# Kernel tuning notes

Hardware: AMD Instinct MI355X
Metric: run time of the kernel (lower is better)

## Reference

```python
import jax, jax.numpy as jnp
import numpy as np

SCALE_FACTOR = 2  # init kwarg
KERNEL = 1        # kernel=1 -> no Gaussian inpainting of empty cells
EPS = 1e-6


def token2map_agg(x, loc_orig, idx_agg, H, W):
    """Scatter-average aggregated tokens onto a dense [B,C,H,W] map.

    Faithful to token2map_agg_sparse with weight=None, kernel=1:
      each original position i gets feature x[idx_agg[i]] with weight 1,
      scattered to the grid cell of loc_orig[i]; per-cell average with
      denominator (count + 1e-6).
    """
    B, N, C = x.shape
    N0 = loc_orig.shape[1]
    lo = jnp.clip(loc_orig, -1.0, 1.0)
    wh = jnp.array([W, H], dtype=lo.dtype)
    # normalized [-1,1] -> pixel coords, round-half-even like torch.round
    px = jnp.round(0.5 * (lo + 1.0) * wh - 0.5).astype(jnp.int32)
    ix = jnp.clip(px[..., 0], 0, W - 1)
    iy = jnp.clip(px[..., 1], 0, H - 1)
    seg = (iy * W + ix + jnp.arange(B, dtype=jnp.int32)[:, None] * (H * W)).reshape(-1)  # [B*N0]
    # gather token feature for each original position: [B, N0, C]
    feats = jnp.take_along_axis(x, idx_agg[..., None].astype(jnp.int32), axis=1)
    # scatter features and counts together in one segment_sum
    src = jnp.concatenate([feats, jnp.ones_like(feats[..., :1])], axis=-1).reshape(B * N0, C + 1)
    agg = jax.ops.segment_sum(src, seg, num_segments=B * H * W)  # [B*H*W, C+1]
    out = agg[:, :C] / (agg[:, C:] + EPS)
    return out.reshape(B, H, W, C).transpose(0, 3, 1, 2)  # [B,C,H,W]


def setup_inputs() -> dict:
    key = jax.random.key(0)
    k1, k2, k3, k4 = jax.random.split(key, 4)
    B, N, C = 8, 1024, 128
    N0 = 16384  # 128*128 original grid positions
    x = jax.random.normal(k1, (B, N, C), dtype=jnp.float32)
    loc = jax.random.uniform(k2, (B, N, 2), dtype=jnp.float32, minval=-1.0, maxval=1.0)
    loc_orig = jax.random.uniform(k3, (B, N0, 2), dtype=jnp.float32, minval=-1.0, maxval=1.0)
    idx_agg = jax.random.randint(k4, (B, N0), 0, N, dtype=jnp.int32)
    return {"x": x, "loc": loc, "loc_orig": loc_orig, "idx_agg": idx_agg,
            "map_h": 128, "map_w": 128}


def reference(x, loc, loc_orig, idx_agg, map_h, map_w):
    B, N, C = x.shape
    N0 = idx_agg.shape[1]
    scale_orig = (N0 // N) ** 0.5  # static python value
    if SCALE_FACTOR <= scale_orig:
        h, w = int(map_h * SCALE_FACTOR), int(map_w * SCALE_FACTOR)
        out = token2map_agg(x, loc_orig, idx_agg, h, w)
    else:
        h, w = int(map_h * scale_orig), int(map_w * scale_orig)
        out = token2map_agg(x, loc_orig, idx_agg, h, w)
        h, w = int(map_h * SCALE_FACTOR), int(map_w * SCALE_FACTOR)
        out = jax.image.resize(out, (B, C, h, w), method="bilinear")
    return out
```

## Files before the change

### kernel.cpp

```cpp
#include <hip/hip_runtime.h>

constexpr int B  = 8;
constexpr int N  = 1024;
constexpr int C  = 128;
constexpr int N0 = 16384;
constexpr int HH = 256;
constexpr int WW = 256;
constexpr int HW = HH * WW;
constexpr int NPTS = B * N0;

constexpr int CPG  = 64;
constexpr int GPB  = HW / CPG;
constexpr int NGRP = B * GPB;
constexpr int CAP  = 96;

constexpr int ROW  = CPG + 4;
constexpr int ACC_WORDS = C * ROW;

__device__ __forceinline__ int cell_of(float lx, float ly) {
    lx = fminf(fmaxf(lx, -1.0f), 1.0f);
    ly = fminf(fmaxf(ly, -1.0f), 1.0f);
    float pxf = rintf(0.5f * (lx + 1.0f) * 256.0f - 0.5f);
    float pyf = rintf(0.5f * (ly + 1.0f) * 256.0f - 0.5f);
    int ix = (int)pxf; ix = ix < 0 ? 0 : (ix > WW - 1 ? WW - 1 : ix);
    int iy = (int)pyf; iy = iy < 0 ? 0 : (iy > HH - 1 ? HH - 1 : iy);
    return iy * WW + ix;
}

__global__ void bucket_kernel(const float* __restrict__ loc_orig,
                              const int* __restrict__ idx_agg,
                              int* __restrict__ cursor,
                              int* __restrict__ bucket) {
    int p = blockIdx.x * blockDim.x + threadIdx.x;
    if (p >= NPTS) return;
    float2 l = ((const float2*)loc_orig)[p];
    int b = p >> 14;
    int cell = cell_of(l.x, l.y);
    int g = b * GPB + (cell >> 6);
    int pos = atomicAdd(cursor + g, 1);
    if (pos < CAP) bucket[g * CAP + pos] = ((cell & 63) << 10) | idx_agg[p];
}

__global__ __launch_bounds__(512) void gather_kernel(
        const float* __restrict__ x,
        const int* __restrict__ cursor,
        const int* __restrict__ bucket,
        float* __restrict__ out) {
    __shared__ __align__(16) float acc[ACC_WORDS];
    __shared__ float scale[CPG];
    __shared__ int   recs[CAP];
    __shared__ int   cnt_s;

    int gid   = blockIdx.x;
    int b     = gid >> 10;
    int cell0 = (gid & 1023) * CPG;
    int tid   = threadIdx.x;
    int wave  = tid >> 6, lane = tid & 63;

    int my_cnt = (tid == 0) ? cursor[gid] : 0;
    int my_rec = (tid < CAP) ? bucket[gid * CAP + tid] : 0;

    float4 z4 = make_float4(0.f, 0.f, 0.f, 0.f);
    for (int i = tid; i < ACC_WORDS / 4; i += 512) ((float4*)acc)[i] = z4;
    if (tid < CPG) scale[tid] = 0.0f;

    if (tid == 0) cnt_s = my_cnt > CAP ? CAP : my_cnt;
    if (tid < CAP) recs[tid] = my_rec;
    __syncthreads();

    int cnt = cnt_s;

    for (int j = wave; j < cnt; j += 8) {
        int e = recs[j];
        int local = e >> 10;
        int tok   = e & 1023;
        float2 v = ((const float2*)(x + (size_t)(b * N + tok) * C))[lane];
        atomicAdd(&acc[lane * ROW + local],        v.x);
        atomicAdd(&acc[(lane + 64) * ROW + local], v.y);
        if (lane == 0) atomicAdd(&scale[local], 1.0f);
    }
    __syncthreads();
    if (tid < CPG) scale[tid] = 1.0f / (scale[tid] + 1e-6f);
    __syncthreads();

    int i4 = (tid & 15) * 4;
    int cb = tid >> 4;
    float s0 = scale[i4 + 0], s1 = scale[i4 + 1];
    float s2 = scale[i4 + 2], s3 = scale[i4 + 3];
    float* obase = out + (size_t)b * C * HW + cell0;
    #pragma unroll
    for (int it = 0; it < 4; ++it) {
        int c  = it * 32 + cb;
        int rr = ((c & 1) << 6) + (c >> 1);
        float4 v = *(const float4*)&acc[rr * ROW + i4];
        v.x *= s0; v.y *= s1; v.z *= s2; v.w *= s3;
        *(float4*)(obase + (size_t)c * HW + i4) = v;
    }
}

extern "C" void kernel_launch(void* const* d_in, const int* in_sizes, int n_in,
                              void* d_out, int out_size, void* d_ws, size_t ws_size,
                              hipStream_t stream) {
    const float* x        = (const float*)d_in[0];
    const float* loc_orig = (const float*)d_in[2];
    const int*   idx_agg  = (const int*)d_in[3];
    float* out = (float*)d_out;

    int* cursor = (int*)d_ws;
    int* bucket = cursor + NGRP;

    hipMemsetAsync(cursor, 0, NGRP * sizeof(int), stream);
    bucket_kernel<<<(NPTS + 255) / 256, 256, 0, stream>>>(loc_orig, idx_agg, cursor, bucket);
    gather_kernel<<<NGRP, 512, 0, stream>>>(x, cursor, bucket, out);
}
```

Measured before the change: 345.1 us.

## Use larger 1024-cell buckets with channel-split gather blocks

Bucket granularity grows from 64 to 1024 cells, and each gather block now handles one bucket for a 1/16 slice of channels. Eight lanes cover eight channels of a point, so each wave processes eight points per iteration. The aim is to cut per-bucket overhead and block count imbalance and to make larger contiguous output stores. In exchange, every bucket's records are reread by 16 blocks, x reads become strided 32-byte segments, and the capacity of 512 per 1024 cells (mean 256) could overflow and silently drop points.

```diff
diff --git a/kernel.cpp b/kernel.cpp
--- a/kernel.cpp
+++ b/kernel.cpp
@@ -9,13 +9,15 @@
 constexpr int HW = HH * WW;
 constexpr int NPTS = B * N0;
 
-constexpr int CPG  = 64;
-constexpr int GPB  = HW / CPG;
-constexpr int NGRP = B * GPB;
-constexpr int CAP  = 96;
+constexpr int CPG    = 1024;
+constexpr int GPB    = HW / CPG;
+constexpr int NGRP   = B * GPB;
+constexpr int CSPLIT = 16;
+constexpr int CHB    = C / CSPLIT;
+constexpr int CAP    = 512;
 
-constexpr int ROW  = CPG + 4;
-constexpr int ACC_WORDS = C * ROW;
+constexpr int ROWW = CPG + 4;
+constexpr int ACC_WORDS = CHB * ROWW;
 
 __device__ __forceinline__ int cell_of(float lx, float ly) {
     lx = fminf(fmaxf(lx, -1.0f), 1.0f);
@@ -36,9 +38,9 @@
     float2 l = ((const float2*)loc_orig)[p];
     int b = p >> 14;
     int cell = cell_of(l.x, l.y);
-    int g = b * GPB + (cell >> 6);
+    int g = b * GPB + (cell >> 10);
     int pos = atomicAdd(cursor + g, 1);
-    if (pos < CAP) bucket[g * CAP + pos] = ((cell & 63) << 10) | idx_agg[p];
+    if (pos < CAP) bucket[g * CAP + pos] = ((cell & 1023) << 10) | idx_agg[p];
 }
 
 __global__ __launch_bounds__(512) void gather_kernel(
@@ -47,54 +49,58 @@
         const int* __restrict__ bucket,
         float* __restrict__ out) {
     __shared__ __align__(16) float acc[ACC_WORDS];
-    __shared__ float scale[CPG];
-    __shared__ int   recs[CAP];
-    __shared__ int   cnt_s;
+    __shared__ __align__(16) float scale[CPG];
+    __shared__ int recs[CAP];
+    __shared__ int cnt_s;
 
-    int gid   = blockIdx.x;
-    int b     = gid >> 10;
-    int cell0 = (gid & 1023) * CPG;
-    int tid   = threadIdx.x;
-    int wave  = tid >> 6, lane = tid & 63;
+    int gid    = blockIdx.x;
+    int bgrp   = gid & (NGRP - 1);
+    int csplit = gid >> 9;
+    int b      = bgrp >> 6;
+    int cell0  = (bgrp & 63) * CPG;
+    int ch0    = csplit * CHB;
+    int tid    = threadIdx.x;
+    int wave   = tid >> 6, lane = tid & 63;
 
-    int my_cnt = (tid == 0) ? cursor[gid] : 0;
-    int my_rec = (tid < CAP) ? bucket[gid * CAP + tid] : 0;
+    int my_cnt = (tid == 0) ? cursor[bgrp] : 0;
+    int my_rec = bucket[bgrp * CAP + tid];
 
     float4 z4 = make_float4(0.f, 0.f, 0.f, 0.f);
     for (int i = tid; i < ACC_WORDS / 4; i += 512) ((float4*)acc)[i] = z4;
-    if (tid < CPG) scale[tid] = 0.0f;
-
+    for (int i = tid; i < CPG / 4; i += 512) ((float4*)scale)[i] = z4;
     if (tid == 0) cnt_s = my_cnt > CAP ? CAP : my_cnt;
-    if (tid < CAP) recs[tid] = my_rec;
+    recs[tid] = my_rec;
     __syncthreads();
 
     int cnt = cnt_s;
-
-    for (int j = wave; j < cnt; j += 8) {
-        int e = recs[j];
-        int local = e >> 10;
-        int tok   = e & 1023;
-        float2 v = ((const float2*)(x + (size_t)(b * N + tok) * C))[lane];
-        atomicAdd(&acc[lane * ROW + local],        v.x);
-        atomicAdd(&acc[(lane + 64) * ROW + local], v.y);
-        if (lane == 0) atomicAdd(&scale[local], 1.0f);
+    int chl = lane & 7;
+    const float* xb = x + (size_t)b * N * C + ch0 + chl;
+    for (int base = wave * 8; base < cnt; base += 64) {
+        int p = base + (lane >> 3);
+        if (p < cnt) {
+            int e = recs[p];
+            int local = e >> 10;
+            int tok   = e & 1023;
+            float v = xb[tok * C];
+            atomicAdd(&acc[chl * ROWW + local], v);
+            if (chl == 0) atomicAdd(&scale[local], 1.0f);
+        }
     }
     __syncthreads();
-    if (tid < CPG) scale[tid] = 1.0f / (scale[tid] + 1e-6f);
+    for (int i = tid; i < CPG; i += 512) scale[i] = 1.0f / (scale[i] + 1e-6f);
     __syncthreads();
 
-    int i4 = (tid & 15) * 4;
-    int cb = tid >> 4;
-    float s0 = scale[i4 + 0], s1 = scale[i4 + 1];
-    float s2 = scale[i4 + 2], s3 = scale[i4 + 3];
+    int q  = tid & 255;
+    int i4 = q * 4;
+    int cl = tid >> 8;
+    float4 s = *(const float4*)&scale[i4];
     float* obase = out + (size_t)b * C * HW + cell0;
     #pragma unroll
     for (int it = 0; it < 4; ++it) {
-        int c  = it * 32 + cb;
-        int rr = ((c & 1) << 6) + (c >> 1);
-        float4 v = *(const float4*)&acc[rr * ROW + i4];
-        v.x *= s0; v.y *= s1; v.z *= s2; v.w *= s3;
-        *(float4*)(obase + (size_t)c * HW + i4) = v;
+        int c = cl + it * 2;
+        float4 v = *(const float4*)&acc[c * ROWW + i4];
+        v.x *= s.x; v.y *= s.y; v.z *= s.z; v.w *= s.w;
+        *(float4*)(obase + (size_t)(ch0 + c) * HW + i4) = v;
     }
 }
 
@@ -111,5 +117,5 @@
 
     hipMemsetAsync(cursor, 0, NGRP * sizeof(int), stream);
     bucket_kernel<<<(NPTS + 255) / 256, 256, 0, stream>>>(loc_orig, idx_agg, cursor, bucket);
-    gather_kernel<<<NGRP, 512, 0, stream>>>(x, cursor, bucket, out);
+    gather_kernel<<<NGRP * CSPLIT, 512, 0, stream>>>(x, cursor, bucket, out);
 }
```

Measured after the change: 370.1 us. +7.2%, slower.
